# Kernel tuning notes

Measured on AMD Instinct MI355X. Metric: run time of the kernel, lower is better.

Reference implementation:

```python
import jax, jax.numpy as jnp
import numpy as np

GROUP_SIZES = [16, 16, 16, 16]
K = 2
TEMPERATURE = 1.0
NEG = float(np.finfo(np.float32).min)  # torch.finfo(dtype).min


def setup_inputs() -> dict:
    key = jax.random.key(0)
    k1, k2, k3 = jax.random.split(key, 3)
    B, S, D, E, G = 8, 4096, 1024, 64, len(GROUP_SIZES)
    x = jax.random.normal(k1, (B, S, D), dtype=jnp.float32)
    W_group = jax.random.normal(k2, (G, D), dtype=jnp.float32) * 0.02
    W_expert = jax.random.normal(k3, (E, D), dtype=jnp.float32) * 0.02
    return {"x": x, "W_group": W_group, "W_expert": W_expert}


def reference(x, W_group, W_expert):
    E = W_expert.shape[0]
    # group id of each expert (contiguous ranges) -- static
    expert_group = jnp.asarray(np.repeat(np.arange(len(GROUP_SIZES)), GROUP_SIZES))  # [E]

    # gate logits (no bias), temperature scaling
    expert_logits = jnp.einsum('bsd,ed->bse', x, W_expert) * (1.0 / TEMPERATURE)  # [B,S,E]
    group_logits = jnp.einsum('bsd,gd->bsg', x, W_group)                          # [B,S,G]
    group_probs = jax.nn.softmax(group_logits, axis=-1)
    g_idx = jnp.argmax(group_probs, axis=-1)                                      # [B,S]

    # mask experts outside the selected group's contiguous range
    mask = expert_group[None, None, :] != g_idx[..., None]                        # [B,S,E] bool
    mdt = mask.astype(expert_logits.dtype)
    masked_logits = mdt * NEG + (1.0 - mdt) * expert_logits

    probs_full = jax.nn.softmax(masked_logits, axis=-1)                           # [B,S,E]
    topk_vals, idx = jax.lax.top_k(masked_logits, K)                              # [B,S,K]
    scores = jax.nn.softmax(topk_vals, axis=-1)

    # aux stats (no_grad in original)
    importance = jax.lax.stop_gradient(jnp.mean(probs_full, axis=(0, 1)))         # [E]
    counts = jnp.zeros((E,), probs_full.dtype).at[idx.reshape(-1)].add(1.0)       # [E]
    load = counts / jnp.maximum(jnp.sum(counts), 1.0)
    return (idx, scores, probs_full, importance, load)
```

## Files before the change

### kernel.cpp

```cpp
#include <hip/hip_runtime.h>
#include <math.h>

#define TOKENS   32768
#define DDIM     1024
#define NBLOCKS  512

#define OFF_SCORES 65536
#define OFF_PROBS  131072
#define OFF_IMP    2228224
#define OFF_LOAD   2228288

typedef __attribute__((ext_vector_type(8))) short  short8;
typedef __attribute__((ext_vector_type(4))) float  f32x4;
typedef __attribute__((ext_vector_type(4))) int    intx4;

__device__ __attribute__((aligned(16))) short wfrag[32 * 5 * 3 * 64 * 8];

__device__ inline unsigned rne_hi(float x) {
  unsigned u = __float_as_uint(x);
  unsigned r = u + 0x7fffu + ((u >> 16) & 1u);
  return r & 0xffff0000u;
}

__device__ inline void split3(const float* xv, short8& f1, short8& f2, short8& f3) {
  int o1[4], o2[4], o3[4];
  #pragma unroll
  for (int p = 0; p < 4; ++p) {
    float x0 = xv[2*p], x1 = xv[2*p+1];
    unsigned h0 = rne_hi(x0), h1 = rne_hi(x1);
    o1[p] = (int)((h0 >> 16) | (h1 & 0xffff0000u));
    float r0 = x0 - __uint_as_float(h0);
    float r1 = x1 - __uint_as_float(h1);
    unsigned g0 = rne_hi(r0), g1 = rne_hi(r1);
    o2[p] = (int)((g0 >> 16) | (g1 & 0xffff0000u));
    float s0 = r0 - __uint_as_float(g0);
    float s1 = r1 - __uint_as_float(g1);
    unsigned w0 = rne_hi(s0), w1 = rne_hi(s1);
    o3[p] = (int)((w0 >> 16) | (w1 & 0xffff0000u));
  }
  intx4 t1 = {o1[0], o1[1], o1[2], o1[3]};
  intx4 t2 = {o2[0], o2[1], o2[2], o2[3]};
  intx4 t3 = {o3[0], o3[1], o3[2], o3[3]};
  f1 = __builtin_bit_cast(short8, t1);
  f2 = __builtin_bit_cast(short8, t2);
  f3 = __builtin_bit_cast(short8, t3);
}

__global__ void prep_kernel(const float* __restrict__ Wg, const float* __restrict__ We) {
  const int nt   = blockIdx.x >> 5;
  const int ks   = blockIdx.x & 31;
  const int lane = threadIdx.x & 63;
  const int row  = nt * 16 + (lane & 15);
  const int k0   = ks * 32 + (lane >> 4) * 8;
  float xv[8];
  #pragma unroll
  for (int j = 0; j < 8; ++j) {
    float v = 0.f;
    if (row < 64)      v = We[(size_t)row * DDIM + k0 + j];
    else if (row < 68) v = Wg[(size_t)(row - 64) * DDIM + k0 + j];
    xv[j] = v;
  }
  short8 f1, f2, f3;
  split3(xv, f1, f2, f3);
  short8* dst = (short8*)wfrag + (((size_t)ks * 5 + nt) * 3) * 64 + lane;
  dst[0]   = f1;
  dst[64]  = f2;
  dst[128] = f3;
}

__global__ __launch_bounds__(256, 2)
void router_kernel(const float* __restrict__ x,
                   float* __restrict__ out,
                   float* __restrict__ ws) {
  __shared__ float el[64 * 88];
  __shared__ int   cnt[64];
  const int tid    = threadIdx.x;
  const int lane   = tid & 63;
  const int wv     = tid >> 6;
  const int tokgrp = wv >> 1;
  const int khalf  = wv & 1;
  const int quad   = lane >> 4;
  const int m      = lane & 15;
  const int tokblk = blockIdx.x * 64;
  const int tok0   = tokblk + tokgrp * 32;

  if (tid < 64) cnt[tid] = 0;

  const float* ap0 = x + (size_t)(tok0 + m) * DDIM + khalf * 512 + quad * 8;
  const float* ap1 = ap0 + (size_t)16 * DDIM;

  f32x4 ahi[2][5], alo[2][5];
  #pragma unroll
  for (int mt = 0; mt < 2; ++mt)
    #pragma unroll
    for (int nt = 0; nt < 5; ++nt) { ahi[mt][nt] = 0.f; alo[mt][nt] = 0.f; }

  for (int ks = 0; ks < 16; ++ks) {
    const float* p0 = ap0 + ks * 32;
    const float* p1 = ap1 + ks * 32;
    float4 a0 = *(const float4*)(p0), a1 = *(const float4*)(p0 + 4);
    float4 a2 = *(const float4*)(p1), a3 = *(const float4*)(p1 + 4);

    const short8* bp = (const short8*)wfrag + ((size_t)(khalf * 16 + ks) * 15) * 64 + lane;
    short8 fb[5][3];
    #pragma unroll
    for (int nt = 0; nt < 5; ++nt) {
      fb[nt][0] = bp[nt * 192];
      fb[nt][1] = bp[nt * 192 + 64];
      fb[nt][2] = bp[nt * 192 + 128];
    }
    short8 fa[2][3];
    {
      float av[8] = {a0.x, a0.y, a0.z, a0.w, a1.x, a1.y, a1.z, a1.w};
      split3(av, fa[0][0], fa[0][1], fa[0][2]);
      float bv[8] = {a2.x, a2.y, a2.z, a2.w, a3.x, a3.y, a3.z, a3.w};
      split3(bv, fa[1][0], fa[1][1], fa[1][2]);
    }
    #pragma unroll
    for (int nt = 0; nt < 5; ++nt)
      #pragma unroll
      for (int mt = 0; mt < 2; ++mt) {
        ahi[mt][nt] = __builtin_amdgcn_mfma_f32_16x16x32_bf16(fa[mt][0], fb[nt][0], ahi[mt][nt], 0, 0, 0);
        f32x4 c = alo[mt][nt];
        c = __builtin_amdgcn_mfma_f32_16x16x32_bf16(fa[mt][0], fb[nt][1], c, 0, 0, 0);
        c = __builtin_amdgcn_mfma_f32_16x16x32_bf16(fa[mt][1], fb[nt][0], c, 0, 0, 0);
        c = __builtin_amdgcn_mfma_f32_16x16x32_bf16(fa[mt][1], fb[nt][1], c, 0, 0, 0);
        c = __builtin_amdgcn_mfma_f32_16x16x32_bf16(fa[mt][0], fb[nt][2], c, 0, 0, 0);
        c = __builtin_amdgcn_mfma_f32_16x16x32_bf16(fa[mt][2], fb[nt][0], c, 0, 0, 0);
        c = __builtin_amdgcn_mfma_f32_16x16x32_bf16(fa[mt][1], fb[nt][2], c, 0, 0, 0);
        c = __builtin_amdgcn_mfma_f32_16x16x32_bf16(fa[mt][2], fb[nt][1], c, 0, 0, 0);
        alo[mt][nt] = c;
      }
  }

  if (khalf == 1) {
    #pragma unroll
    for (int mt = 0; mt < 2; ++mt)
      #pragma unroll
      for (int nt = 0; nt < 5; ++nt)
        #pragma unroll
        for (int r = 0; r < 4; ++r)
          el[(tokgrp * 32 + mt * 16 + quad * 4 + r) * 88 + nt * 16 + m] =
              ahi[mt][nt][r] + alo[mt][nt][r];
  }
  __syncthreads();
  if (khalf == 0) {
    #pragma unroll
    for (int mt = 0; mt < 2; ++mt)
      #pragma unroll
      for (int nt = 0; nt < 5; ++nt)
        #pragma unroll
        for (int r = 0; r < 4; ++r) {
          const int idx = (tokgrp * 32 + mt * 16 + quad * 4 + r) * 88 + nt * 16 + m;
          el[idx] += ahi[mt][nt][r] + alo[mt][nt][r];
        }
  }
  __syncthreads();

  if (tid < 64) {
    const int t = tid;
    float* row = el + t * 88;
    const float g0 = row[64], g1 = row[65], g2 = row[66], g3 = row[67];
    int g = 0; float gb = g0;
    if (g1 > gb) { g = 1; gb = g1; }
    if (g2 > gb) { g = 2; gb = g2; }
    if (g3 > gb) { g = 3; gb = g3; }
    const int base = g << 4;
    float l[16];
    #pragma unroll
    for (int e = 0; e < 16; ++e) l[e] = row[base + e];
    int i1 = 0; float v1 = l[0];
    #pragma unroll
    for (int e = 1; e < 16; ++e) if (l[e] > v1) { i1 = e; v1 = l[e]; }
    int i2 = -1; float v2 = 0.f;
    #pragma unroll
    for (int e = 0; e < 16; ++e) {
      if (e == i1) continue;
      if (i2 < 0 || l[e] > v2) { i2 = e; v2 = l[e]; }
    }
    float pr[16]; float s = 0.f;
    #pragma unroll
    for (int e = 0; e < 16; ++e) { pr[e] = expf(l[e] - v1); s += pr[e]; }
    const float inv = 1.f / s;
    #pragma unroll
    for (int c = 0; c < 64; ++c) row[c] = 0.f;
    #pragma unroll
    for (int e = 0; e < 16; ++e) row[base + e] = pr[e] * inv;
    const size_t T = (size_t)tokblk + t;
    out[2*T]     = (float)(base + i1);
    out[2*T + 1] = (float)(base + i2);
    const float e2 = expf(v2 - v1);
    const float si = 1.f / (1.f + e2);
    out[OFF_SCORES + 2*T]     = si;
    out[OFF_SCORES + 2*T + 1] = e2 * si;
    atomicAdd(&cnt[base + i1], 1);
    atomicAdd(&cnt[base + i2], 1);
  }
  __syncthreads();

  for (int i = tid; i < 64 * 64; i += 256) {
    const int t = i >> 6, c = i & 63;
    out[OFF_PROBS + (((size_t)(tokblk + t)) << 6) + c] = el[t * 88 + c];
  }
  if (tid < 64) {
    const int e = tid;
    float s = 0.f;
    for (int t = 0; t < 64; ++t) s += el[t * 88 + e];
    atomicAdd(&ws[e], s);
    atomicAdd(&ws[64 + e], (float)cnt[e]);
  }
}

__global__ void finalize_kernel(const float* __restrict__ ws, float* __restrict__ out) {
  const int e = threadIdx.x;
  if (e < 64) {
    out[OFF_IMP  + e] = ws[e]      * (1.0f / 32768.0f);
    out[OFF_LOAD + e] = ws[64 + e] * (1.0f / 65536.0f);
  }
}

extern "C" void kernel_launch(void* const* d_in, const int* in_sizes, int n_in,
                              void* d_out, int out_size, void* d_ws, size_t ws_size,
                              hipStream_t stream) {
  (void)in_sizes; (void)n_in; (void)out_size; (void)ws_size;
  const float* x  = (const float*)d_in[0];
  const float* Wg = (const float*)d_in[1];
  const float* We = (const float*)d_in[2];
  float* out = (float*)d_out;
  float* ws  = (float*)d_ws;
  hipMemsetAsync(d_ws, 0, 128 * sizeof(float), stream);
  hipLaunchKernelGGL(prep_kernel, dim3(160), dim3(64), 0, stream, Wg, We);
  hipLaunchKernelGGL(router_kernel, dim3(NBLOCKS), dim3(256), 0, stream, x, out, ws);
  hipLaunchKernelGGL(finalize_kernel, dim3(1), dim3(64), 0, stream, ws, out);
}
```

Before: 221.7 us.

## Shrink router blocks to 16 tokens and spread stat atomics across slots

Each router block now handles 16 tokens with two waves, each wave covering one K half, instead of 64 tokens with four waves. The grid grows from 512 to 2048 blocks so there are more blocks in flight across the CUs. Importance and count atomics go to 16 separate slots that finalize sums, which spreads contention on the global accumulators. Each B fragment is now reused by only one M tile instead of two, so weight-fragment loads per token double, and there are more block-level syncs and atomics overall.

```diff
diff --git a/kernel.cpp b/kernel.cpp
--- a/kernel.cpp
+++ b/kernel.cpp
@@ -3,12 +3,15 @@
 
 #define TOKENS   32768
 #define DDIM     1024
-#define NBLOCKS  512
+#define TPB      16
+#define NBLOCKS  (TOKENS / TPB)
 
 #define OFF_SCORES 65536
 #define OFF_PROBS  131072
 #define OFF_IMP    2228224
 #define OFF_LOAD   2228288
+
+#define NSLOT 16
 
 typedef __attribute__((ext_vector_type(8))) short  short8;
 typedef __attribute__((ext_vector_type(4))) float  f32x4;
@@ -68,38 +71,30 @@
   dst[128] = f3;
 }
 
-__global__ __launch_bounds__(256, 2)
+__global__ __launch_bounds__(128, 4)
 void router_kernel(const float* __restrict__ x,
                    float* __restrict__ out,
                    float* __restrict__ ws) {
-  __shared__ float el[64 * 88];
-  __shared__ int   cnt[64];
+  __shared__ __attribute__((aligned(16))) float el[TPB * 88];
+  __shared__ int cnt[64];
   const int tid    = threadIdx.x;
   const int lane   = tid & 63;
-  const int wv     = tid >> 6;
-  const int tokgrp = wv >> 1;
-  const int khalf  = wv & 1;
+  const int khalf  = tid >> 6;
   const int quad   = lane >> 4;
   const int m      = lane & 15;
-  const int tokblk = blockIdx.x * 64;
-  const int tok0   = tokblk + tokgrp * 32;
+  const int tokblk = blockIdx.x * TPB;
 
   if (tid < 64) cnt[tid] = 0;
 
-  const float* ap0 = x + (size_t)(tok0 + m) * DDIM + khalf * 512 + quad * 8;
-  const float* ap1 = ap0 + (size_t)16 * DDIM;
-
-  f32x4 ahi[2][5], alo[2][5];
+  const float* ap0 = x + (size_t)(tokblk + m) * DDIM + khalf * 512 + quad * 8;
+
+  f32x4 ahi[5], alo[5];
   #pragma unroll
-  for (int mt = 0; mt < 2; ++mt)
-    #pragma unroll
-    for (int nt = 0; nt < 5; ++nt) { ahi[mt][nt] = 0.f; alo[mt][nt] = 0.f; }
+  for (int nt = 0; nt < 5; ++nt) { ahi[nt] = 0.f; alo[nt] = 0.f; }
 
   for (int ks = 0; ks < 16; ++ks) {
     const float* p0 = ap0 + ks * 32;
-    const float* p1 = ap1 + ks * 32;
     float4 a0 = *(const float4*)(p0), a1 = *(const float4*)(p0 + 4);
-    float4 a2 = *(const float4*)(p1), a3 = *(const float4*)(p1 + 4);
 
     const short8* bp = (const short8*)wfrag + ((size_t)(khalf * 16 + ks) * 15) * 64 + lane;
     short8 fb[5][3];
@@ -109,55 +104,46 @@
       fb[nt][1] = bp[nt * 192 + 64];
       fb[nt][2] = bp[nt * 192 + 128];
     }
-    short8 fa[2][3];
+    short8 fa[3];
     {
       float av[8] = {a0.x, a0.y, a0.z, a0.w, a1.x, a1.y, a1.z, a1.w};
-      split3(av, fa[0][0], fa[0][1], fa[0][2]);
-      float bv[8] = {a2.x, a2.y, a2.z, a2.w, a3.x, a3.y, a3.z, a3.w};
-      split3(bv, fa[1][0], fa[1][1], fa[1][2]);
-    }
+      split3(av, fa[0], fa[1], fa[2]);
+    }
+    #pragma unroll
+    for (int nt = 0; nt < 5; ++nt) {
+      ahi[nt] = __builtin_amdgcn_mfma_f32_16x16x32_bf16(fa[0], fb[nt][0], ahi[nt], 0, 0, 0);
+      f32x4 c = alo[nt];
+      c = __builtin_amdgcn_mfma_f32_16x16x32_bf16(fa[0], fb[nt][1], c, 0, 0, 0);
+      c = __builtin_amdgcn_mfma_f32_16x16x32_bf16(fa[1], fb[nt][0], c, 0, 0, 0);
+      c = __builtin_amdgcn_mfma_f32_16x16x32_bf16(fa[1], fb[nt][1], c, 0, 0, 0);
+      c = __builtin_amdgcn_mfma_f32_16x16x32_bf16(fa[0], fb[nt][2], c, 0, 0, 0);
+      c = __builtin_amdgcn_mfma_f32_16x16x32_bf16(fa[2], fb[nt][0], c, 0, 0, 0);
+      c = __builtin_amdgcn_mfma_f32_16x16x32_bf16(fa[1], fb[nt][2], c, 0, 0, 0);
+      c = __builtin_amdgcn_mfma_f32_16x16x32_bf16(fa[2], fb[nt][1], c, 0, 0, 0);
+      alo[nt] = c;
+    }
+  }
+
+  if (khalf == 1) {
     #pragma unroll
     for (int nt = 0; nt < 5; ++nt)
       #pragma unroll
-      for (int mt = 0; mt < 2; ++mt) {
-        ahi[mt][nt] = __builtin_amdgcn_mfma_f32_16x16x32_bf16(fa[mt][0], fb[nt][0], ahi[mt][nt], 0, 0, 0);
-        f32x4 c = alo[mt][nt];
-        c = __builtin_amdgcn_mfma_f32_16x16x32_bf16(fa[mt][0], fb[nt][1], c, 0, 0, 0);
-        c = __builtin_amdgcn_mfma_f32_16x16x32_bf16(fa[mt][1], fb[nt][0], c, 0, 0, 0);
-        c = __builtin_amdgcn_mfma_f32_16x16x32_bf16(fa[mt][1], fb[nt][1], c, 0, 0, 0);
-        c = __builtin_amdgcn_mfma_f32_16x16x32_bf16(fa[mt][0], fb[nt][2], c, 0, 0, 0);
-        c = __builtin_amdgcn_mfma_f32_16x16x32_bf16(fa[mt][2], fb[nt][0], c, 0, 0, 0);
-        c = __builtin_amdgcn_mfma_f32_16x16x32_bf16(fa[mt][1], fb[nt][2], c, 0, 0, 0);
-        c = __builtin_amdgcn_mfma_f32_16x16x32_bf16(fa[mt][2], fb[nt][1], c, 0, 0, 0);
-        alo[mt][nt] = c;
-      }
-  }
-
-  if (khalf == 1) {
-    #pragma unroll
-    for (int mt = 0; mt < 2; ++mt)
-      #pragma unroll
-      for (int nt = 0; nt < 5; ++nt)
-        #pragma unroll
-        for (int r = 0; r < 4; ++r)
-          el[(tokgrp * 32 + mt * 16 + quad * 4 + r) * 88 + nt * 16 + m] =
-              ahi[mt][nt][r] + alo[mt][nt][r];
+      for (int r = 0; r < 4; ++r)
+        el[(quad * 4 + r) * 88 + nt * 16 + m] = ahi[nt][r] + alo[nt][r];
   }
   __syncthreads();
   if (khalf == 0) {
     #pragma unroll
-    for (int mt = 0; mt < 2; ++mt)
+    for (int nt = 0; nt < 5; ++nt)
       #pragma unroll
-      for (int nt = 0; nt < 5; ++nt)
-        #pragma unroll
-        for (int r = 0; r < 4; ++r) {
-          const int idx = (tokgrp * 32 + mt * 16 + quad * 4 + r) * 88 + nt * 16 + m;
-          el[idx] += ahi[mt][nt][r] + alo[mt][nt][r];
-        }
+      for (int r = 0; r < 4; ++r) {
+        const int idx = (quad * 4 + r) * 88 + nt * 16 + m;
+        el[idx] += ahi[nt][r] + alo[nt][r];
+      }
   }
   __syncthreads();
 
-  if (tid < 64) {
+  if (tid < TPB) {
     const int t = tid;
     float* row = el + t * 88;
     const float g0 = row[64], g1 = row[65], g2 = row[66], g3 = row[67];
@@ -198,24 +184,32 @@
   }
   __syncthreads();
 
-  for (int i = tid; i < 64 * 64; i += 256) {
+  for (int i = tid; i < TPB * 64; i += 128) {
     const int t = i >> 6, c = i & 63;
     out[OFF_PROBS + (((size_t)(tokblk + t)) << 6) + c] = el[t * 88 + c];
   }
   if (tid < 64) {
     const int e = tid;
     float s = 0.f;
-    for (int t = 0; t < 64; ++t) s += el[t * 88 + e];
-    atomicAdd(&ws[e], s);
-    atomicAdd(&ws[64 + e], (float)cnt[e]);
+    #pragma unroll 4
+    for (int t = 0; t < TPB; ++t) s += el[t * 88 + e];
+    const int slot = (blockIdx.x & (NSLOT - 1)) * 128;
+    atomicAdd(&ws[slot + e], s);
+    atomicAdd(&ws[slot + 64 + e], (float)cnt[e]);
   }
 }
 
 __global__ void finalize_kernel(const float* __restrict__ ws, float* __restrict__ out) {
   const int e = threadIdx.x;
   if (e < 64) {
-    out[OFF_IMP  + e] = ws[e]      * (1.0f / 32768.0f);
-    out[OFF_LOAD + e] = ws[64 + e] * (1.0f / 65536.0f);
+    float imp = 0.f, cf = 0.f;
+    #pragma unroll
+    for (int s = 0; s < NSLOT; ++s) {
+      imp += ws[s * 128 + e];
+      cf  += ws[s * 128 + 64 + e];
+    }
+    out[OFF_IMP  + e] = imp * (1.0f / 32768.0f);
+    out[OFF_LOAD + e] = cf  * (1.0f / 65536.0f);
   }
 }
 
@@ -228,8 +222,8 @@
   const float* We = (const float*)d_in[2];
   float* out = (float*)d_out;
   float* ws  = (float*)d_ws;
-  hipMemsetAsync(d_ws, 0, 128 * sizeof(float), stream);
+  hipMemsetAsync(d_ws, 0, NSLOT * 128 * sizeof(float), stream);
   hipLaunchKernelGGL(prep_kernel, dim3(160), dim3(64), 0, stream, Wg, We);
-  hipLaunchKernelGGL(router_kernel, dim3(NBLOCKS), dim3(256), 0, stream, x, out, ws);
+  hipLaunchKernelGGL(router_kernel, dim3(NBLOCKS), dim3(128), 0, stream, x, out, ws);
   hipLaunchKernelGGL(finalize_kernel, dim3(1), dim3(64), 0, stream, ws, out);
 }
```

After: 243.4 us. 1.1x slower.
